# Optimization experiments

Measured on AMD Instinct MI355X. Metric: run time of the kernel, lower is better.

## Reference

```python
import jax, jax.numpy as jnp
import numpy as np

DIM = 256; QK = 256; HEADS = 8; TOPK = 2; WV = 2; WH = 2
SCALE = QK ** -0.5


def setup_inputs() -> dict:
    key = jax.random.key(0)
    ks = jax.random.split(key, 6)
    x = jax.random.normal(ks[0], (4, DIM, 64, 64), jnp.float32)
    Wqkv = jax.random.normal(ks[1], (DIM, 2 * QK + DIM), jnp.float32) * 0.02
    bqkv = jnp.zeros((2 * QK + DIM,), jnp.float32)
    Wo = jax.random.normal(ks[2], (DIM, DIM), jnp.float32) * 0.02
    bo = jnp.zeros((DIM,), jnp.float32)
    lepe_w = jax.random.normal(ks[3], (3, 3, 1, DIM), jnp.float32) * 0.1  # HWIO depthwise
    lepe_b = jnp.zeros((DIM,), jnp.float32)
    return {"x": x, "Wqkv": Wqkv, "bqkv": bqkv, "Wo": Wo, "bo": bo,
            "lepe_w": lepe_w, "lepe_b": lepe_b}


def _dwconv(x, w, b):
    # depthwise 3x3 conv, NHWC
    y = jax.lax.conv_general_dilated(x, w, (1, 1), 'SAME',
                                     dimension_numbers=('NHWC', 'HWIO', 'NHWC'),
                                     feature_group_count=x.shape[-1])
    return y + b


def _branch(win, Wqkv, bqkv, lepe_w, lepe_b, to_image):
    n, p2, h, w, _ = win.shape
    w2 = h * w
    qkv = win @ Wqkv + bqkv
    q = qkv[..., :QK]
    kv = qkv[..., QK:]                                  # [n,p2,h,w,QK+DIM]
    q_pix = q.reshape(n, p2, w2, QK)
    kv_pix = kv.reshape(n, p2, w2, QK + DIM)            # identity kv_down
    # region routing (detached in original)
    q_win = jax.lax.stop_gradient(q).mean((2, 3))       # [n,p2,QK]
    k_win = jax.lax.stop_gradient(kv[..., :QK]).mean((2, 3))
    logit = jnp.einsum('npc,nqc->npq', q_win * SCALE, k_win)
    _, r_idx = jax.lax.top_k(logit, TOPK)               # [n,p2,TOPK]
    # gather selected KV windows (mul_weight='none')
    kv_sel = jax.vmap(lambda kvb, idxb: kvb[idxb])(kv_pix, r_idx)  # [n,p2,k,w2,ckv]
    k_sel = kv_sel[..., :QK].reshape(n, p2, TOPK * w2, HEADS, QK // HEADS)
    v_sel = kv_sel[..., QK:].reshape(n, p2, TOPK * w2, HEADS, DIM // HEADS)
    qh = q_pix.reshape(n, p2, w2, HEADS, QK // HEADS)
    attn = jax.nn.softmax(jnp.einsum('npqhd,npkhd->nphqk', qh * SCALE, k_sel), axis=-1)
    out = jnp.einsum('nphqk,npkhd->npqhd', attn, v_sel).reshape(n, p2, h, w, DIM)
    lepe = _dwconv(to_image(kv[..., QK:]), lepe_w, lepe_b)
    return to_image(out) + lepe


def reference(x, Wqkv, bqkv, Wo, bo, lepe_w, lepe_b):
    xh = x.transpose(0, 2, 3, 1)                        # NHWC
    N, H, W, C = xh.shape
    v_win, h_win = H // WV, W // WH
    # vertical branch: horizontal strips of height WV, full width
    vm = xh.reshape(N, v_win, WV, W, C)
    # horizontal branch: vertical strips of width WH, full height
    hm = xh.reshape(N, H, h_win, WH, C).transpose(0, 2, 1, 3, 4)
    img_v = lambda a: a.reshape(N, H, W, a.shape[-1])
    img_h = lambda a: a.transpose(0, 2, 1, 3, 4).reshape(N, H, W, a.shape[-1])
    o1 = _branch(vm, Wqkv, bqkv, lepe_w, lepe_b, img_v)
    o2 = _branch(hm, Wqkv, bqkv, lepe_w, lepe_b, img_h)
    out = (o1 @ Wo + bo) + (o2 @ Wo + bo)
    return out.transpose(0, 3, 1, 2)                    # back to NCHW
```

## Files before the change

kernel.cpp:

```cpp
#include <hip/hip_runtime.h>
#include <hip/hip_bf16.h>
#include <math.h>

#define NBATCH 4
#define HW     4096
#define NPIX   16384
#define SCALE  0.0625f
#define QLOG2E (0.0625f * 1.44269504088896340736f)

typedef __attribute__((ext_vector_type(8))) short bf16x8;
typedef __attribute__((ext_vector_type(4))) float f32x4;

__device__ __forceinline__ int pixmap(int b, int n, int p, int pos){
  return (b == 0) ? (n*HW + p*128 + pos)
                  : (n*HW + (pos >> 1)*64 + (p << 1) + (pos & 1));
}

__device__ __forceinline__ ushort f2b(float x){
  __hip_bfloat16 h = __float2bfloat16(x);
  return *reinterpret_cast<ushort*>(&h);
}
__device__ __forceinline__ float b2f(ushort u){
  __hip_bfloat16 h = *reinterpret_cast<__hip_bfloat16*>(&u);
  return __bfloat162float(h);
}
__device__ __forceinline__ uint pk2(float a, float b){
  return (uint)f2b(a) | ((uint)f2b(b) << 16);
}

__global__ __launch_bounds__(256) void k_xt(
    const float* __restrict__ x, ushort* __restrict__ Xb)
{
  __shared__ float T[32][257];
  const int n = blockIdx.y, hw0 = blockIdx.x * 32;
  const int tid = threadIdx.x;
  const int hl = tid & 31, cg = tid >> 5;
  #pragma unroll 8
  for(int i = 0; i < 32; i++){
    const int c = i*8 + cg;
    T[hl][c] = x[((size_t)(n*256 + c))*4096 + hw0 + hl];
  }
  __syncthreads();
  const int c0 = (tid & 31)*8, pb = tid >> 5;
  #pragma unroll
  for(int i = 0; i < 4; i++){
    const int p = pb + 8*i;
    union { bf16x8 v; ushort u[8]; } U;
    #pragma unroll
    for(int j = 0; j < 8; j++) U.u[j] = f2b(T[p][c0 + j]);
    *(bf16x8*)(Xb + ((size_t)(n*HW + hw0 + p))*256 + c0) = U.v;
  }
}

__global__ __launch_bounds__(256) void k_wt(
    const float* __restrict__ Wqkv, ushort* __restrict__ Wt)
{
  const int o = blockIdx.x, t = threadIdx.x;
  Wt[(size_t)o*256 + t] = f2b(Wqkv[(size_t)t*768 + o]);
}

__global__ __launch_bounds__(256) void k_wto(
    const float* __restrict__ Wo, ushort* __restrict__ WoT)
{
  const int o = blockIdx.x, t = threadIdx.x;
  WoT[(size_t)o*256 + t] = f2b(Wo[(size_t)t*256 + o]);
}

__global__ __launch_bounds__(256) void k_qkv_mfma(
    const ushort* __restrict__ Xb, const ushort* __restrict__ Wt,
    const float* __restrict__ bqkv, ushort* __restrict__ QKVb,
    ushort* __restrict__ Vt)
{
  const int tid = threadIdx.x;
  const int l = tid & 63, w = tid >> 6;
  const int wr = w >> 1, wc = w & 1;
  const int q16 = l & 15, g = l >> 4;
  const int row0 = blockIdx.x*128 + wr*64;
  const int col0 = blockIdx.y*128 + wc*64;

  f32x4 acc[4][4];
  #pragma unroll
  for(int i = 0; i < 4; i++)
    #pragma unroll
    for(int j = 0; j < 4; j++) acc[i][j] = (f32x4){0,0,0,0};

  const ushort* Ab = Xb + (size_t)(row0 + q16)*256 + 8*g;
  const ushort* Bb = Wt + (size_t)(col0 + q16)*256 + 8*g;

  #pragma unroll
  for(int ks = 0; ks < 8; ks++){
    const int k0 = ks*32;
    bf16x8 a[4], b[4];
    #pragma unroll
    for(int i = 0; i < 4; i++) a[i] = *(const bf16x8*)(Ab + (size_t)(16*i)*256 + k0);
    #pragma unroll
    for(int j = 0; j < 4; j++) b[j] = *(const bf16x8*)(Bb + (size_t)(16*j)*256 + k0);
    #pragma unroll
    for(int i = 0; i < 4; i++)
      #pragma unroll
      for(int j = 0; j < 4; j++)
        acc[i][j] = __builtin_amdgcn_mfma_f32_16x16x32_bf16(a[i], b[j], acc[i][j], 0, 0, 0);
  }

  const int n = row0 >> 12, hwb = row0 & 4095;
  #pragma unroll
  for(int j = 0; j < 4; j++){
    const int col = col0 + 16*j + q16;
    const float bias = bqkv[col];
    const float sc = (col < 256) ? QLOG2E : 1.f;
    #pragma unroll
    for(int i = 0; i < 4; i++){
      ushort4 u;
      u.x = f2b((acc[i][j][0] + bias) * sc);
      u.y = f2b((acc[i][j][1] + bias) * sc);
      u.z = f2b((acc[i][j][2] + bias) * sc);
      u.w = f2b((acc[i][j][3] + bias) * sc);
      const int row = row0 + 16*i + 4*g;
      QKVb[(size_t)(row+0)*768 + col] = u.x;
      QKVb[(size_t)(row+1)*768 + col] = u.y;
      QKVb[(size_t)(row+2)*768 + col] = u.z;
      QKVb[(size_t)(row+3)*768 + col] = u.w;
      if(col >= 512){
        *(ushort4*)&Vt[((size_t)(n*256 + col - 512))*4096 + hwb + 16*i + 4*g] = u;
      }
    }
  }
}

__global__ __launch_bounds__(256) void k_xmean(
    const float* __restrict__ x, float* __restrict__ xwin)
{
  const int n = blockIdx.y;
  const int c = blockIdx.x*4 + (threadIdx.x >> 6);
  const int l = threadIdx.x & 63;
  const float* xc = x + ((size_t)(n*256 + c))*4096;

  float4 cs[8];
  #pragma unroll
  for(int i = 0; i < 8; i++) cs[i] = (float4){0,0,0,0};
  float rsum = 0.f;
  const float4* xr = (const float4*)(xc + l*64);
  #pragma unroll
  for(int i = 0; i < 16; i++){
    const float4 v = xr[i];
    rsum += (v.x+v.y)+(v.z+v.w);
    const float p0 = v.x+v.y, p1 = v.z+v.w;
    if(i & 1){ cs[i>>1].z += p0; cs[i>>1].w += p1; }
    else     { cs[i>>1].x += p0; cs[i>>1].y += p1; }
  }
  #pragma unroll
  for(int i = 0; i < 8; i++){
    #pragma unroll
    for(int sb = 0; sb < 6; sb++){
      const int s = 1 << sb;
      cs[i].x += __shfl_xor(cs[i].x, s);
      cs[i].y += __shfl_xor(cs[i].y, s);
      cs[i].z += __shfl_xor(cs[i].z, s);
      cs[i].w += __shfl_xor(cs[i].w, s);
    }
  }
  const int p = l & 31;
  const float rp = __shfl(rsum, 2*p) + __shfl(rsum, 2*p + 1);
  float cp;
  {
    const int hi = p >> 2, lo = p & 3;
    const float4 q = hi==0?cs[0]:hi==1?cs[1]:hi==2?cs[2]:hi==3?cs[3]
                   : hi==4?cs[4]:hi==5?cs[5]:hi==6?cs[6]:cs[7];
    cp = lo==0?q.x : lo==1?q.y : lo==2?q.z : q.w;
  }
  if(l < 32){
    xwin[((size_t)((0*NBATCH + n)*32 + p))*256 + c] = rp * (1.f/128.f);
    xwin[((size_t)((1*NBATCH + n)*32 + p))*256 + c] = cp * (1.f/128.f);
  }
}

__global__ __launch_bounds__(256) void k_win_gemm(
    const float* __restrict__ xwin, const float* __restrict__ Wqkv,
    const float* __restrict__ bqkv, float* __restrict__ qwin, float* __restrict__ kwin)
{
  __shared__ float xs[256];
  const int row = blockIdx.x;
  const int tid = threadIdx.x;
  xs[tid] = xwin[(size_t)row*256 + tid];
  __syncthreads();
  #pragma unroll
  for(int half = 0; half < 2; half++){
    const int col = half*256 + tid;
    float s = 0.f;
    for(int k = 0; k < 256; k++) s += xs[k] * Wqkv[(size_t)k*768 + col];
    s += bqkv[col];
    if(half == 0) qwin[(size_t)row*256 + tid] = s;
    else          kwin[(size_t)row*256 + tid] = s;
  }
}

__global__ __launch_bounds__(256) void k_logits_top2(
    const float* __restrict__ qwin, const float* __restrict__ kwin, int* __restrict__ ridx)
{
  const int n = blockIdx.x, b = blockIdx.y;
  __shared__ float lg[32][32];
  const int base = ((b*NBATCH + n)*32)*256;
  for(int t = threadIdx.x; t < 1024; t += 256){
    const int p = t >> 5, q = t & 31;
    const float* qp = qwin + base + p*256;
    const float* kq = kwin + base + q*256;
    float s = 0.f;
    for(int c = 0; c < 256; c++) s += qp[c]*kq[c];
    lg[p][q] = s * SCALE;
  }
  __syncthreads();
  if(threadIdx.x < 32){
    const int p = threadIdx.x;
    float m0 = -INFINITY; int i0 = 0;
    for(int q = 0; q < 32; q++){ const float v = lg[p][q]; if(v > m0){ m0 = v; i0 = q; } }
    float m1 = -INFINITY; int i1 = 0;
    for(int q = 0; q < 32; q++){ if(q == i0) continue; const float v = lg[p][q]; if(v > m1){ m1 = v; i1 = q; } }
    const int o = ((b*NBATCH + n)*32 + p)*2;
    ridx[o] = i0; ridx[o+1] = i1;
  }
}

struct KVFrag { bf16x8 kf0, kf1, vf0, vf1; };

__device__ __forceinline__ KVFrag load_kv(
    const ushort* __restrict__ QKVb, const ushort* __restrict__ Vt,
    int b, int n, int wsel, int posb, int hd, int q16, int g)
{
  KVFrag f;
  const int kp0 = pixmap(b, n, wsel, posb + q16);
  f.kf0 = *(const bf16x8*)(QKVb + (size_t)kp0*768 + 256 + hd*32 + 8*g);
  const int kp1 = pixmap(b, n, wsel, posb + 16 + q16);
  f.kf1 = *(const bf16x8*)(QKVb + (size_t)kp1*768 + 256 + hd*32 + 8*g);
  if(b == 0){
    const ushort* base = Vt + ((size_t)(n*256 + hd*32 + q16))*4096 + wsel*128 + posb + 4*g;
    union { bf16x8 v; ushort4 h[2]; } U0, U1;
    U0.h[0] = *(const ushort4*)(base);
    U0.h[1] = *(const ushort4*)(base + 16);
    U1.h[0] = *(const ushort4*)(base + (size_t)16*4096);
    U1.h[1] = *(const ushort4*)(base + (size_t)16*4096 + 16);
    f.vf0 = U0.v; f.vf1 = U1.v;
  } else {
    const int h0 = (posb + 4*g) >> 1;
    const ushort* base = Vt + ((size_t)(n*256 + hd*32 + q16))*4096 + 2*wsel;
    union { bf16x8 v; uint u[4]; } U0, U1;
    U0.u[0] = *(const uint*)(base + (h0    )*64);
    U0.u[1] = *(const uint*)(base + (h0 + 1)*64);
    U0.u[2] = *(const uint*)(base + (h0 + 8)*64);
    U0.u[3] = *(const uint*)(base + (h0 + 9)*64);
    const ushort* base1 = base + (size_t)16*4096;
    U1.u[0] = *(const uint*)(base1 + (h0    )*64);
    U1.u[1] = *(const uint*)(base1 + (h0 + 1)*64);
    U1.u[2] = *(const uint*)(base1 + (h0 + 8)*64);
    U1.u[3] = *(const uint*)(base1 + (h0 + 9)*64);
    f.vf0 = U0.v; f.vf1 = U1.v;
  }
  return f;
}

__global__ __launch_bounds__(256) void k_attn_mfma(
    const ushort* __restrict__ QKVb, const ushort* __restrict__ Vt,
    const int* __restrict__ ridx, ushort* __restrict__ Ob)
{
  int id = blockIdx.x*4 + (threadIdx.x >> 6);
  const int hd = id & 7;  id >>= 3;
  const int p  = id & 31; id >>= 5;
  const int n  = id & 3;  id >>= 2;
  const int b  = id;
  const int l = threadIdx.x & 63;
  const int q16 = l & 15, g = l >> 4;

  const int ro = ((b*NBATCH + n)*32 + p)*2;
  const int r0 = ridx[ro], r1 = ridx[ro+1];

  int qpix[8];
  bf16x8 qf[8];
  #pragma unroll
  for(int m = 0; m < 8; m++){
    qpix[m] = pixmap(b, n, p, m*16 + q16);
    qf[m] = *(const bf16x8*)(QKVb + (size_t)qpix[m]*768 + hd*32 + 8*g);
  }

  f32x4 acc0[8], acc1[8];
  float rs[8];
  #pragma unroll
  for(int m = 0; m < 8; m++){
    acc0[m] = (f32x4){0,0,0,0}; acc1[m] = (f32x4){0,0,0,0}; rs[m] = 0.f;
  }

  #define COMPUTE(F)                                                            \
    _Pragma("unroll")                                                           \
    for(int m = 0; m < 8; m++){                                                 \
      const f32x4 z = {0,0,0,0};                                                \
      f32x4 s0 = __builtin_amdgcn_mfma_f32_16x16x32_bf16((F).kf0, qf[m], z, 0, 0, 0); \
      f32x4 s1 = __builtin_amdgcn_mfma_f32_16x16x32_bf16((F).kf1, qf[m], z, 0, 0, 0); \
      const float e00 = exp2f(s0[0]), e01 = exp2f(s0[1]), e02 = exp2f(s0[2]), e03 = exp2f(s0[3]); \
      const float e10 = exp2f(s1[0]), e11 = exp2f(s1[1]), e12 = exp2f(s1[2]), e13 = exp2f(s1[3]); \
      rs[m] += ((e00+e01)+(e02+e03)) + ((e10+e11)+(e12+e13));                   \
      union { bf16x8 v; uint u[4]; } P;                                         \
      P.u[0] = pk2(e00, e01);                                                   \
      P.u[1] = pk2(e02, e03);                                                   \
      P.u[2] = pk2(e10, e11);                                                   \
      P.u[3] = pk2(e12, e13);                                                   \
      acc0[m] = __builtin_amdgcn_mfma_f32_16x16x32_bf16((F).vf0, P.v, acc0[m], 0, 0, 0); \
      acc1[m] = __builtin_amdgcn_mfma_f32_16x16x32_bf16((F).vf1, P.v, acc1[m], 0, 0, 0); \
    }

  KVFrag fA = load_kv(QKVb, Vt, b, n, r0, 0, hd, q16, g);
  for(int cc = 0; cc < 8; cc += 2){
    const int w1 = (cc+1 < 4) ? r0 : r1;
    KVFrag fB = load_kv(QKVb, Vt, b, n, w1, (32*(cc+1)) & 127, hd, q16, g);
    COMPUTE(fA);
    if(cc + 2 < 8){
      const int w2 = (cc+2 < 4) ? r0 : r1;
      fA = load_kv(QKVb, Vt, b, n, w2, (32*(cc+2)) & 127, hd, q16, g);
    }
    COMPUTE(fB);
  }
  #undef COMPUTE

  #pragma unroll
  for(int m = 0; m < 8; m++){
    float r = rs[m];
    r += __shfl_xor(r, 16);
    r += __shfl_xor(r, 32);
    rs[m] = 1.f / r;
  }
  #pragma unroll
  for(int m = 0; m < 8; m++){
    ushort* op = Ob + ((size_t)b*NPIX + qpix[m])*256 + hd*32 + 4*g;
    const float iv = rs[m];
    ushort4 o0 = { f2b(acc0[m][0]*iv), f2b(acc0[m][1]*iv), f2b(acc0[m][2]*iv), f2b(acc0[m][3]*iv) };
    ushort4 o1 = { f2b(acc1[m][0]*iv), f2b(acc1[m][1]*iv), f2b(acc1[m][2]*iv), f2b(acc1[m][3]*iv) };
    *(ushort4*)op = o0;
    *(ushort4*)(op + 16) = o1;
  }
}

__global__ __launch_bounds__(256) void k_combine_lepe(
    const ushort* __restrict__ QKVb, const ushort* __restrict__ Ob0,
    const ushort* __restrict__ Ob1,
    const float* __restrict__ lw, const float* __restrict__ lb, ushort* __restrict__ Sb)
{
  const int pix = blockIdx.x;
  const int c = threadIdx.x;
  const int n = pix >> 12, rem = pix & 4095;
  const int h = rem >> 6, w = rem & 63;
  float conv = 0.f;
  #pragma unroll
  for(int kh = 0; kh < 3; kh++){
    const int hh = h + kh - 1;
    if(hh < 0 || hh >= 64) continue;
    #pragma unroll
    for(int kw = 0; kw < 3; kw++){
      const int wi = w + kw - 1;
      if(wi < 0 || wi >= 64) continue;
      const int np = (n*64 + hh)*64 + wi;
      conv += b2f(QKVb[(size_t)np*768 + 512 + c]) * lw[(kh*3 + kw)*256 + c];
    }
  }
  const size_t idx = (size_t)pix*256 + c;
  Sb[idx] = f2b(b2f(Ob0[idx]) + b2f(Ob1[idx]) + 2.f*(conv + lb[c]));
}

__global__ __launch_bounds__(256) void k_out_mfma(
    const ushort* __restrict__ Sb, const ushort* __restrict__ WoT,
    const float* __restrict__ bo, float* __restrict__ out)
{
  const int tid = threadIdx.x;
  const int l = tid & 63, w = tid >> 6;
  const int wr = w >> 1, wc = w & 1;
  const int q16 = l & 15, g = l >> 4;
  const int c0   = blockIdx.x*128 + wr*64;
  const int pix0 = blockIdx.y*128 + wc*64;
  const int n = pix0 >> 12, rem0 = pix0 & 4095;

  f32x4 acc[4][4];
  #pragma unroll
  for(int i = 0; i < 4; i++)
    #pragma unroll
    for(int j = 0; j < 4; j++) acc[i][j] = (f32x4){0,0,0,0};

  const ushort* Ab = WoT + (size_t)(c0 + q16)*256 + 8*g;
  const ushort* Bb = Sb  + (size_t)(pix0 + q16)*256 + 8*g;

  #pragma unroll
  for(int ks = 0; ks < 8; ks++){
    const int k0 = ks*32;
    bf16x8 a[4], b[4];
    #pragma unroll
    for(int i = 0; i < 4; i++) a[i] = *(const bf16x8*)(Ab + (size_t)(16*i)*256 + k0);
    #pragma unroll
    for(int j = 0; j < 4; j++) b[j] = *(const bf16x8*)(Bb + (size_t)(16*j)*256 + k0);
    #pragma unroll
    for(int i = 0; i < 4; i++)
      #pragma unroll
      for(int j = 0; j < 4; j++)
        acc[i][j] = __builtin_amdgcn_mfma_f32_16x16x32_bf16(a[i], b[j], acc[i][j], 0, 0, 0);
  }

  float* outn = out + (size_t)n*256*4096;
  #pragma unroll
  for(int i = 0; i < 4; i++){
    #pragma unroll
    for(int r = 0; r < 4; r++){
      const int c = c0 + 16*i + 4*g + r;
      const float bias = 2.f*bo[c];
      #pragma unroll
      for(int j = 0; j < 4; j++){
        const int rem = rem0 + 16*j + q16;
        outn[(size_t)c*4096 + rem] = acc[i][j][r] + bias;
      }
    }
  }
}

extern "C" void kernel_launch(void* const* d_in, const int* in_sizes, int n_in,
                              void* d_out, int out_size, void* d_ws, size_t ws_size,
                              hipStream_t stream)
{
  const float* x    = (const float*)d_in[0];
  const float* Wqkv = (const float*)d_in[1];
  const float* bqkv = (const float*)d_in[2];
  const float* Wo   = (const float*)d_in[3];
  const float* bo   = (const float*)d_in[4];
  const float* lw   = (const float*)d_in[5];
  const float* lb   = (const float*)d_in[6];
  float* out = (float*)d_out;

  char* w = (char*)d_ws;
  ushort* Xb   = (ushort*)w; w += (size_t)NPIX*256*2;
  ushort* Wt   = (ushort*)w; w += (size_t)768*256*2;
  ushort* WoT  = (ushort*)w; w += (size_t)256*256*2;
  ushort* QKVb = (ushort*)w; w += (size_t)NPIX*768*2;
  ushort* Vt   = (ushort*)w; w += (size_t)NPIX*256*2;
  ushort* Ob   = (ushort*)w; w += (size_t)2*NPIX*256*2;
  ushort* Sb   = (ushort*)w; w += (size_t)NPIX*256*2;
  float*  xwin = (float*)w;  w += (size_t)2*NBATCH*32*256*4;
  float*  qwin = (float*)w;  w += (size_t)2*NBATCH*32*256*4;
  float*  kwin = (float*)w;  w += (size_t)2*NBATCH*32*256*4;
  int*    ridx = (int*)w;    w += (size_t)2*NBATCH*32*2*4;

  ushort* Ob0 = Ob;
  ushort* Ob1 = Ob + (size_t)NPIX*256;

  k_xt          <<<dim3(128,NBATCH), 256, 0, stream>>>(x, Xb);
  k_wt          <<<768, 256, 0, stream>>>(Wqkv, Wt);
  k_wto         <<<256, 256, 0, stream>>>(Wo, WoT);
  k_qkv_mfma    <<<dim3(128,6), 256, 0, stream>>>(Xb, Wt, bqkv, QKVb, Vt);
  k_xmean       <<<dim3(64,NBATCH), 256, 0, stream>>>(x, xwin);
  k_win_gemm    <<<256, 256, 0, stream>>>(xwin, Wqkv, bqkv, qwin, kwin);
  k_logits_top2 <<<dim3(NBATCH,2), 256, 0, stream>>>(qwin, kwin, ridx);
  k_attn_mfma   <<<512, 256, 0, stream>>>(QKVb, Vt, ridx, Ob);
  k_combine_lepe<<<NPIX, 256, 0, stream>>>(QKVb, Ob0, Ob1, lw, lb, Sb);
  k_out_mfma    <<<dim3(2,128), 256, 0, stream>>>(Sb, WoT, bo, out);
}
```

Baseline: 186.3 us.

## Truncate softmax probabilities to bf16, raise wave priority, merge weight-prep kernels

The attention kernel now packs exp values into bf16 by truncating the upper 16 bits instead of round-to-nearest conversion. This cuts the VALU instruction count in the softmax inner loop. The compute block is also wrapped in s_setprio to favour MFMA/exp waves over waves issuing loads. Separately, the two weight transpose kernels are merged into one launch to save launch overhead. Truncation adds a small bias in the probability values used for the PV product.

```diff
diff --git a/kernel.cpp b/kernel.cpp
--- a/kernel.cpp
+++ b/kernel.cpp
@@ -24,8 +24,8 @@
   __hip_bfloat16 h = *reinterpret_cast<__hip_bfloat16*>(&u);
   return __bfloat162float(h);
 }
-__device__ __forceinline__ uint pk2(float a, float b){
-  return (uint)f2b(a) | ((uint)f2b(b) << 16);
+__device__ __forceinline__ uint pk2t(float a, float b){
+  return (__float_as_uint(a) >> 16) | (__float_as_uint(b) & 0xFFFF0000u);
 }
 
 __global__ __launch_bounds__(256) void k_xt(
@@ -52,18 +52,17 @@
   }
 }
 
-__global__ __launch_bounds__(256) void k_wt(
-    const float* __restrict__ Wqkv, ushort* __restrict__ Wt)
+__global__ __launch_bounds__(256) void k_wprep(
+    const float* __restrict__ Wqkv, const float* __restrict__ Wo,
+    ushort* __restrict__ Wt, ushort* __restrict__ WoT)
 {
   const int o = blockIdx.x, t = threadIdx.x;
-  Wt[(size_t)o*256 + t] = f2b(Wqkv[(size_t)t*768 + o]);
-}
-
-__global__ __launch_bounds__(256) void k_wto(
-    const float* __restrict__ Wo, ushort* __restrict__ WoT)
-{
-  const int o = blockIdx.x, t = threadIdx.x;
-  WoT[(size_t)o*256 + t] = f2b(Wo[(size_t)t*256 + o]);
+  if(o < 768){
+    Wt[(size_t)o*256 + t] = f2b(Wqkv[(size_t)t*768 + o]);
+  } else {
+    const int c = o - 768;
+    WoT[(size_t)c*256 + t] = f2b(Wo[(size_t)t*256 + c]);
+  }
 }
 
 __global__ __launch_bounds__(256) void k_qkv_mfma(
@@ -288,6 +287,7 @@
   }
 
   #define COMPUTE(F)                                                            \
+    __builtin_amdgcn_s_setprio(1);                                              \
     _Pragma("unroll")                                                           \
     for(int m = 0; m < 8; m++){                                                 \
       const f32x4 z = {0,0,0,0};                                                \
@@ -297,13 +297,14 @@
       const float e10 = exp2f(s1[0]), e11 = exp2f(s1[1]), e12 = exp2f(s1[2]), e13 = exp2f(s1[3]); \
       rs[m] += ((e00+e01)+(e02+e03)) + ((e10+e11)+(e12+e13));                   \
       union { bf16x8 v; uint u[4]; } P;                                         \
-      P.u[0] = pk2(e00, e01);                                                   \
-      P.u[1] = pk2(e02, e03);                                                   \
-      P.u[2] = pk2(e10, e11);                                                   \
-      P.u[3] = pk2(e12, e13);                                                   \
+      P.u[0] = pk2t(e00, e01);                                                  \
+      P.u[1] = pk2t(e02, e03);                                                  \
+      P.u[2] = pk2t(e10, e11);                                                  \
+      P.u[3] = pk2t(e12, e13);                                                  \
       acc0[m] = __builtin_amdgcn_mfma_f32_16x16x32_bf16((F).vf0, P.v, acc0[m], 0, 0, 0); \
       acc1[m] = __builtin_amdgcn_mfma_f32_16x16x32_bf16((F).vf1, P.v, acc1[m], 0, 0, 0); \
-    }
+    }                                                                           \
+    __builtin_amdgcn_s_setprio(0);
 
   KVFrag fA = load_kv(QKVb, Vt, b, n, r0, 0, hd, q16, g);
   for(int cc = 0; cc < 8; cc += 2){
@@ -444,8 +445,7 @@
   ushort* Ob1 = Ob + (size_t)NPIX*256;
 
   k_xt          <<<dim3(128,NBATCH), 256, 0, stream>>>(x, Xb);
-  k_wt          <<<768, 256, 0, stream>>>(Wqkv, Wt);
-  k_wto         <<<256, 256, 0, stream>>>(Wo, WoT);
+  k_wprep       <<<1024, 256, 0, stream>>>(Wqkv, Wo, Wt, WoT);
   k_qkv_mfma    <<<dim3(128,6), 256, 0, stream>>>(Xb, Wt, bqkv, QKVb, Vt);
   k_xmean       <<<dim3(64,NBATCH), 256, 0, stream>>>(x, xwin);
   k_win_gemm    <<<256, 256, 0, stream>>>(xwin, Wqkv, bqkv, qwin, kwin);
```

Measured after the change: 182.3 us. -2.2%, faster.
